# Kernel optimization log

Hardware: AMD Instinct MI355X
Metric: run time of the kernel (lower is better)

## Reference

```python
import jax, jax.numpy as jnp
import numpy as np

N, E, R = 50000, 320000, 3
IN, HID, OUT = 768, 256, 64
NEG_SLOPE = 0.2


def _rgat_conv(x, src, dst, edge_type, W, q, k, bias):
    # x: [N, HID]; W: [R, HID, HID]; q,k: [HID, 1]; bias: [HID]
    n = x.shape[0]
    xw = jnp.einsum('nc,rco->rno', x, W)          # [R, N, HID] per-relation transform
    out_i = xw[edge_type, dst]                      # [E, HID] transformed target feats
    out_j = xw[edge_type, src]                      # [E, HID] transformed source feats
    alpha = jax.nn.leaky_relu(out_i @ q + out_j @ k, NEG_SLOPE)  # [E, 1]
    # across-relation segment softmax over destination nodes (PyG softmax semantics)
    m = jax.ops.segment_max(alpha, dst, num_segments=n)          # [N, 1]
    ea = jnp.exp(alpha - m[dst])
    denom = jax.ops.segment_sum(ea, dst, num_segments=n)         # [N, 1]
    a = ea / (denom[dst] + 1e-16)                                # [E, 1]
    out = jax.ops.segment_sum(a * out_j, dst, num_segments=n)    # [N, HID]
    return out + bias


def setup_inputs() -> dict:
    key = jax.random.key(0)
    ks = jax.random.split(key, 16)
    g = lambda k, shape, fan: (jax.random.normal(k, shape, jnp.float32) / np.float32(np.sqrt(fan)))
    return {
        'x': jax.random.normal(ks[0], (N, IN), jnp.float32),
        'edge_index': jax.random.randint(ks[1], (2, E), 0, N),
        'edge_type': jax.random.randint(ks[2], (E,), 0, R),
        'w_in': g(ks[3], (IN, HID), IN), 'b_in': jnp.zeros((HID,), jnp.float32),
        'conv1_w': g(ks[4], (R, HID, HID), HID),
        'conv1_q': g(ks[5], (HID, 1), HID),
        'conv1_k': g(ks[6], (HID, 1), HID),
        'conv1_b': jnp.zeros((HID,), jnp.float32),
        'conv2_w': g(ks[7], (R, HID, HID), HID),
        'conv2_q': g(ks[8], (HID, 1), HID),
        'conv2_k': g(ks[9], (HID, 1), HID),
        'conv2_b': jnp.zeros((HID,), jnp.float32),
        'w_out': g(ks[10], (HID, OUT), HID), 'b_out': jnp.zeros((OUT,), jnp.float32),
        'w_cls': g(ks[11], (OUT, 2), OUT), 'b_cls': jnp.zeros((2,), jnp.float32),
    }


def reference(x, edge_index, edge_type, w_in, b_in,
              conv1_w, conv1_q, conv1_k, conv1_b,
              conv2_w, conv2_q, conv2_k, conv2_b,
              w_out, b_out, w_cls, b_cls):
    src, dst = edge_index[0], edge_index[1]
    h = jax.nn.relu(x @ w_in + b_in)                                  # [N, HID]
    h = _rgat_conv(h, src, dst, edge_type, conv1_w, conv1_q, conv1_k, conv1_b)
    h = _rgat_conv(h, src, dst, edge_type, conv2_w, conv2_q, conv2_k, conv2_b)
    h = jax.nn.relu(h @ w_out + b_out)                                # [N, OUT]
    return h @ w_cls + b_cls                                          # [N, 2]
```

## Files before the change

kernel.cpp:

```cpp
#include <hip/hip_runtime.h>
#include <hip/hip_bf16.h>

#define RG86_NN 50000
#define RG86_NE 320000
#define RG86_NR 3
#define RG86_DIN 768
#define RG86_HID 256
#define RG86_OUT 64

typedef __bf16 rg_bv8 __attribute__((ext_vector_type(8)));
typedef short rg_sv8 __attribute__((ext_vector_type(8)));
typedef float rg_fv4 __attribute__((ext_vector_type(4)));
typedef unsigned int rg_u32;

static __device__ float rg_b2f(unsigned short u) {
  return __uint_as_float(((unsigned int)u) << 16);
}
static __device__ unsigned short rg_f2b(float f) {
  unsigned int u = __float_as_uint(f);
  u += 0x7FFFu + ((u >> 16) & 1u);
  return (unsigned short)(u >> 16);
}

static __device__ __forceinline__ void rg_gl16(const void* g, void* lds_wave_base) {
  __builtin_amdgcn_global_load_lds(
      (const __attribute__((address_space(1))) rg_u32*)(unsigned long long)(uintptr_t)g,
      (__attribute__((address_space(3))) rg_u32*)(unsigned int)(uintptr_t)lds_wave_base,
      16, 0, 0);
}

__global__ void RGATModel_86371792322702_kernel() {}

__global__ void rg_cast(const float* in, unsigned short* out, int n) {
  int i = (blockIdx.x * 256 + threadIdx.x) * 4;
  if (i < n) {
    float4 v = *(const float4*)(in + i);
    ushort4 o = make_ushort4(rg_f2b(v.x), rg_f2b(v.y), rg_f2b(v.z), rg_f2b(v.w));
    *(ushort4*)(out + i) = o;
  }
}

__global__ void rg_castT(const float* in, unsigned short* out, int rows, int cols) {
  int i = blockIdx.x * 256 + threadIdx.x;
  if (i < rows * cols) {
    int r = i / cols, c = i % cols;
    out[(size_t)c * rows + r] = rg_f2b(in[i]);
  }
}

__global__ void rg_castT3(const float* in, unsigned short* out) {
  int i = blockIdx.x * 256 + threadIdx.x;
  if (i < RG86_NR * RG86_HID * RG86_HID) {
    int r = i >> 16, j = i & 65535;
    int row = j >> 8, col = j & 255;
    out[(r << 16) + (col << 8) + row] = rg_f2b(in[i]);
  }
}

__global__ __launch_bounds__(256) void rg_gemm2(
    const unsigned short* A, const unsigned short* Bt, const float* bias,
    unsigned short* C, int M, int N, int K, int relu, int split) {
  __shared__ unsigned short sA[128 * 64];
  __shared__ unsigned short sB[64 * 64];
  int tid = threadIdx.x;
  int wv = tid >> 6, lane = tid & 63;
  int nwg = gridDim.x;
  int q = nwg >> 3, rres = nwg & 7;
  int xcd = blockIdx.x & 7, jj = blockIdx.x >> 3;
  int wg = (xcd < rres ? xcd * (q + 1) : rres * (q + 1) + (xcd - rres) * q) + jj;
  int ntiles = N >> 6;
  int mt = wg / ntiles, nt = wg - mt * ntiles;
  int m0 = mt * 128, n0 = nt * 64;
  int frow = lane & 15, fhi = lane >> 4;
  rg_fv4 acc[2][4] = {};
  for (int k0 = 0; k0 < K; k0 += 64) {
#pragma unroll
    for (int i = 0; i < 4; i++) {
      int idx = i * 256 + tid;
      int r = idx >> 3, s = idx & 7;
      int gr = m0 + r;
      if (gr >= M) gr = M - 1;
      const unsigned short* gp = A + (size_t)gr * K + k0 + ((s ^ (r & 7)) << 3);
      rg_gl16(gp, (char*)sA + (size_t)(i * 256 + wv * 64) * 16);
    }
#pragma unroll
    for (int i = 0; i < 2; i++) {
      int idx = i * 256 + tid;
      int r = idx >> 3, s = idx & 7;
      const unsigned short* gp = Bt + (size_t)(n0 + r) * K + k0 + ((s ^ (r & 7)) << 3);
      rg_gl16(gp, (char*)sB + (size_t)(i * 256 + wv * 64) * 16);
    }
    __syncthreads();
#pragma unroll
    for (int ks = 0; ks < 2; ks++) {
      rg_bv8 af[2], bf[4];
#pragma unroll
      for (int mf = 0; mf < 2; mf++) {
        int r = wv * 32 + mf * 16 + frow;
        int slot = (ks * 4 + fhi) ^ (r & 7);
        af[mf] = *(const rg_bv8*)((const char*)sA + r * 128 + slot * 16);
      }
#pragma unroll
      for (int nf = 0; nf < 4; nf++) {
        int r = nf * 16 + frow;
        int slot = (ks * 4 + fhi) ^ (r & 7);
        bf[nf] = *(const rg_bv8*)((const char*)sB + r * 128 + slot * 16);
      }
#pragma unroll
      for (int mf = 0; mf < 2; mf++)
#pragma unroll
        for (int nf = 0; nf < 4; nf++)
          acc[mf][nf] = __builtin_amdgcn_mfma_f32_16x16x32_bf16(af[mf], bf[nf],
                                                                acc[mf][nf], 0, 0, 0);
    }
    __syncthreads();
  }
#pragma unroll
  for (int mf = 0; mf < 2; mf++) {
#pragma unroll
    for (int nf = 0; nf < 4; nf++) {
      int col = n0 + nf * 16 + frow;
      float bv = bias ? bias[col] : 0.f;
#pragma unroll
      for (int r = 0; r < 4; r++) {
        int row = m0 + wv * 32 + mf * 16 + fhi * 4 + r;
        if (row < M) {
          float v = acc[mf][nf][r] + bv;
          if (relu && v < 0.f) v = 0.f;
          if (split)
            C[((size_t)(col >> 8) * RG86_NN + row) * 256 + (col & 255)] = rg_f2b(v);
          else
            C[(size_t)row * N + col] = rg_f2b(v);
        }
      }
    }
  }
}

__global__ void rg_hist(const int* d, int* counts) {
  int e = blockIdx.x * 256 + threadIdx.x;
  if (e < RG86_NE) atomicAdd(&counts[d[e]], 1);
}

__global__ void rg_scan1(const int* counts, int* tmp, int* bsum, int n) {
  int b = blockIdx.x, t = threadIdx.x;
  int base = b * 1024 + t * 4;
  int v0 = 0, v1 = 0, v2 = 0, v3 = 0;
  if (base + 3 < n) {
    int4 v = *(const int4*)(counts + base);
    v0 = v.x; v1 = v.y; v2 = v.z; v3 = v.w;
  } else {
    if (base + 0 < n) v0 = counts[base + 0];
    if (base + 1 < n) v1 = counts[base + 1];
    if (base + 2 < n) v2 = counts[base + 2];
    if (base + 3 < n) v3 = counts[base + 3];
  }
  int tsum = v0 + v1 + v2 + v3;
  int lane = t & 63, wave = t >> 6;
  int s = tsum;
  for (int off = 1; off < 64; off <<= 1) {
    int u = __shfl_up(s, off);
    if (lane >= off) s += u;
  }
  __shared__ int wsum[4];
  if (lane == 63) wsum[wave] = s;
  __syncthreads();
  int woff = 0;
  for (int w = 0; w < wave; w++) woff += wsum[w];
  int excl = woff + s - tsum;
  int e0 = excl, e1 = e0 + v0, e2 = e1 + v1, e3 = e2 + v2;
  if (base + 3 < n) {
    *(int4*)(tmp + base) = make_int4(e0, e1, e2, e3);
  } else {
    if (base + 0 < n) tmp[base + 0] = e0;
    if (base + 1 < n) tmp[base + 1] = e1;
    if (base + 2 < n) tmp[base + 2] = e2;
    if (base + 3 < n) tmp[base + 3] = e3;
  }
  if (t == 255) bsum[b] = woff + s;
}

__global__ void rg_scan2(int* bsum, int* rowptr, int nb, int n) {
  int lane = threadIdx.x;
  int v = (lane < nb) ? bsum[lane] : 0;
  int s = v;
  for (int off = 1; off < 64; off <<= 1) {
    int u = __shfl_up(s, off);
    if (lane >= off) s += u;
  }
  if (lane < nb) bsum[lane] = s - v;
  if (lane == 63) rowptr[n] = s;
}

__global__ void rg_scan3(const int* bsum, int* rowptr, int* cursor, int n) {
  int b = blockIdx.x, t = threadIdx.x;
  int base = b * 1024 + t * 4;
  int off = bsum[b];
  if (base + 3 < n) {
    int4 v = *(const int4*)(cursor + base);
    int4 o = make_int4(v.x + off, v.y + off, v.z + off, v.w + off);
    *(int4*)(rowptr + base) = o;
    *(int4*)(cursor + base) = o;
  } else {
    for (int j = 0; j < 4; j++)
      if (base + j < n) {
        int o = cursor[base + j] + off;
        rowptr[base + j] = o;
        cursor[base + j] = o;
      }
  }
}

__global__ void rg_scatter(const int* d, int* cursor, int* perm) {
  int e = blockIdx.x * 256 + threadIdx.x;
  if (e < RG86_NE) perm[atomicAdd(&cursor[d[e]], 1)] = e;
}

__global__ void rg_qk(const unsigned short* xw, const float* q, const float* k,
                      float* qd, float* kd) {
  int lane = threadIdx.x & 63;
  int p = blockIdx.x * 4 + (threadIdx.x >> 6);
  if (p >= RG86_NR * RG86_NN) return;
  const unsigned short* xr = xw + (size_t)p * RG86_HID + lane * 4;
  float qv = 0.f, kv = 0.f;
  for (int j = 0; j < 4; j++) {
    float xv = rg_b2f(xr[j]);
    qv += xv * q[lane * 4 + j];
    kv += xv * k[lane * 4 + j];
  }
  for (int o = 32; o >= 1; o >>= 1) { qv += __shfl_xor(qv, o); kv += __shfl_xor(kv, o); }
  if (lane == 0) { qd[p] = qv; kd[p] = kv; }
}

__global__ void rg_edge(const int* perm, const int* src, const int* dst,
                        const int* et, const float* qd, const float* kd,
                        float* alphap, int* srcrel) {
  int i = blockIdx.x * 256 + threadIdx.x;
  if (i >= RG86_NE) return;
  int e = perm[i];
  int t = et[e], sv = src[e], dv = dst[e];
  float al = qd[t * RG86_NN + dv] + kd[t * RG86_NN + sv];
  al = al > 0.f ? al : 0.2f * al;
  alphap[i] = al;
  srcrel[i] = t * RG86_NN + sv;
}

__global__ void rg_agg(const int* rowptr, const float* alphap, const int* srcrel,
                       const unsigned short* xw, const float* bias,
                       unsigned short* out) {
  __shared__ float sw[4][64];
  __shared__ int ssrc[4][64];
  int lane = threadIdx.x & 63;
  int wv = threadIdx.x >> 6;
  int node = blockIdx.x * 4 + wv;
  if (node >= RG86_NN) return;
  int s0 = rowptr[node], s1 = rowptr[node + 1];
  int c0 = lane * 4;
  float a0 = 0.f, a1 = 0.f, a2 = 0.f, a3 = 0.f;
  if (s1 > s0) {
    float m = -1e30f;
    for (int bs = s0; bs < s1; bs += 64) {
      int i = bs + lane;
      float al = (i < s1) ? alphap[i] : -1e30f;
      m = fmaxf(m, al);
    }
    for (int o = 32; o >= 1; o >>= 1) m = fmaxf(m, __shfl_xor(m, o));
    float den = 0.f;
    for (int bs = s0; bs < s1; bs += 64) {
      int i = bs + lane;
      if (i < s1) den += __expf(alphap[i] - m);
    }
    for (int o = 32; o >= 1; o >>= 1) den += __shfl_xor(den, o);
    float inv = 1.f / (den + 1e-16f);
    for (int bs = s0; bs < s1; bs += 64) {
      int i = bs + lane;
      int nch = s1 - bs; if (nch > 64) nch = 64;
      float w = 0.f; int sr = 0;
      if (i < s1) { w = __expf(alphap[i] - m) * inv; sr = srcrel[i]; }
      sw[wv][lane] = w;
      ssrc[wv][lane] = sr;
#pragma unroll 4
      for (int j = 0; j < nch; j++) {
        float wj = sw[wv][j];
        ushort4 v = *(const ushort4*)(xw + (size_t)ssrc[wv][j] * RG86_HID + c0);
        a0 += wj * rg_b2f(v.x);
        a1 += wj * rg_b2f(v.y);
        a2 += wj * rg_b2f(v.z);
        a3 += wj * rg_b2f(v.w);
      }
    }
  }
  unsigned short* op = out + (size_t)node * RG86_HID + c0;
  op[0] = rg_f2b(a0 + bias[c0 + 0]);
  op[1] = rg_f2b(a1 + bias[c0 + 1]);
  op[2] = rg_f2b(a2 + bias[c0 + 2]);
  op[3] = rg_f2b(a3 + bias[c0 + 3]);
}

__global__ void rg_cls(const unsigned short* h4, const float* wc, const float* bc,
                       float* out) {
  int n = blockIdx.x * 256 + threadIdx.x;
  if (n >= RG86_NN) return;
  float a0 = bc[0], a1 = bc[1];
  const unsigned short* hr = h4 + (size_t)n * RG86_OUT;
  for (int j = 0; j < RG86_OUT; j++) {
    float h = rg_b2f(hr[j]);
    a0 += h * wc[j * 2 + 0];
    a1 += h * wc[j * 2 + 1];
  }
  out[n * 2 + 0] = a0;
  out[n * 2 + 1] = a1;
}

extern "C" void kernel_launch(void* const* d_in, const int* in_sizes, int n_in,
                              void* d_out, int out_size, void* d_ws, size_t ws_size,
                              hipStream_t stream) {
  (void)in_sizes; (void)n_in; (void)out_size;
  const float* x = (const float*)d_in[0];
  const int* ei = (const int*)d_in[1];
  const int* etp = (const int*)d_in[2];
  const float* w_in = (const float*)d_in[3];
  const float* b_in = (const float*)d_in[4];
  const float* c1w = (const float*)d_in[5];
  const float* c1q = (const float*)d_in[6];
  const float* c1k = (const float*)d_in[7];
  const float* c1b = (const float*)d_in[8];
  const float* c2w = (const float*)d_in[9];
  const float* c2q = (const float*)d_in[10];
  const float* c2k = (const float*)d_in[11];
  const float* c2b = (const float*)d_in[12];
  const float* w_out = (const float*)d_in[13];
  const float* b_out = (const float*)d_in[14];
  const float* w_cls = (const float*)d_in[15];
  const float* b_cls = (const float*)d_in[16];
  const int* esrc = ei;
  const int* edst = ei + RG86_NE;

  char* base = (char*)d_ws;
  size_t off = 0;
  unsigned short* xb = (unsigned short*)(base + off);
  unsigned short* xw = xb;
  off += (size_t)RG86_NN * RG86_DIN * 2;
  unsigned short* h1b = (unsigned short*)(base + off); off += (size_t)RG86_NN * RG86_HID * 2;
  unsigned short* h2b = (unsigned short*)(base + off); off += (size_t)RG86_NN * RG86_HID * 2;
  unsigned short* h4b = (unsigned short*)(base + off); off += (size_t)RG86_NN * RG86_OUT * 2;
  unsigned short* w_inT = (unsigned short*)(base + off); off += (size_t)RG86_DIN * RG86_HID * 2;
  unsigned short* c1wT = (unsigned short*)(base + off); off += (size_t)RG86_NR * RG86_HID * RG86_HID * 2;
  unsigned short* c2wT = (unsigned short*)(base + off); off += (size_t)RG86_NR * RG86_HID * RG86_HID * 2;
  unsigned short* w_outT = (unsigned short*)(base + off); off += (size_t)RG86_HID * RG86_OUT * 2;
  float* qd = (float*)(base + off); off += (size_t)RG86_NR * RG86_NN * 4;
  float* kd = (float*)(base + off); off += (size_t)RG86_NR * RG86_NN * 4;
  int* counts = (int*)(base + off); off += (size_t)RG86_NN * 4;
  int* rowptr = (int*)(base + off); off += (size_t)(RG86_NN + 4) * 4;
  int* cursor = (int*)(base + off); off += (size_t)RG86_NN * 4;
  int* perm = (int*)(base + off); off += (size_t)RG86_NE * 4;
  int* bsum = (int*)(base + off); off += (size_t)64 * 4;
  float* alphap = (float*)(base + off); off += (size_t)RG86_NE * 4;
  int* srcrel = (int*)(base + off); off += (size_t)RG86_NE * 4;
  if (off > ws_size) return;

  int mt128 = (RG86_NN + 127) / 128;
  int nsb = (RG86_NN + 1023) / 1024;

  rg_cast<<<(RG86_NN * RG86_DIN / 4 + 255) / 256, 256, 0, stream>>>(
      x, xb, RG86_NN * RG86_DIN);
  rg_castT<<<(RG86_DIN * RG86_HID + 255) / 256, 256, 0, stream>>>(
      w_in, w_inT, RG86_DIN, RG86_HID);
  rg_castT3<<<(RG86_NR * RG86_HID * RG86_HID + 255) / 256, 256, 0, stream>>>(c1w, c1wT);
  rg_castT3<<<(RG86_NR * RG86_HID * RG86_HID + 255) / 256, 256, 0, stream>>>(c2w, c2wT);
  rg_castT<<<(RG86_HID * RG86_OUT + 255) / 256, 256, 0, stream>>>(
      w_out, w_outT, RG86_HID, RG86_OUT);

  rg_gemm2<<<mt128 * 4, 256, 0, stream>>>(xb, w_inT, b_in, h1b,
                                          RG86_NN, RG86_HID, RG86_DIN, 1, 0);

  hipMemsetAsync(counts, 0, (size_t)RG86_NN * 4, stream);
  rg_hist<<<(RG86_NE + 255) / 256, 256, 0, stream>>>(edst, counts);
  rg_scan1<<<nsb, 256, 0, stream>>>(counts, cursor, bsum, RG86_NN);
  rg_scan2<<<1, 64, 0, stream>>>(bsum, rowptr, nsb, RG86_NN);
  rg_scan3<<<nsb, 256, 0, stream>>>(bsum, rowptr, cursor, RG86_NN);
  rg_scatter<<<(RG86_NE + 255) / 256, 256, 0, stream>>>(edst, cursor, perm);

  rg_gemm2<<<mt128 * 12, 256, 0, stream>>>(h1b, c1wT, (const float*)0, xw,
                                           RG86_NN, RG86_NR * RG86_HID, RG86_HID, 0, 1);
  rg_qk<<<(RG86_NR * RG86_NN + 3) / 4, 256, 0, stream>>>(xw, c1q, c1k, qd, kd);
  rg_edge<<<(RG86_NE + 255) / 256, 256, 0, stream>>>(perm, esrc, edst, etp, qd, kd,
                                                     alphap, srcrel);
  rg_agg<<<(RG86_NN + 3) / 4, 256, 0, stream>>>(rowptr, alphap, srcrel,
                                                xw, c1b, h2b);

  rg_gemm2<<<mt128 * 12, 256, 0, stream>>>(h2b, c2wT, (const float*)0, xw,
                                           RG86_NN, RG86_NR * RG86_HID, RG86_HID, 0, 1);
  rg_qk<<<(RG86_NR * RG86_NN + 3) / 4, 256, 0, stream>>>(xw, c2q, c2k, qd, kd);
  rg_edge<<<(RG86_NE + 255) / 256, 256, 0, stream>>>(perm, esrc, edst, etp, qd, kd,
                                                     alphap, srcrel);
  rg_agg<<<(RG86_NN + 3) / 4, 256, 0, stream>>>(rowptr, alphap, srcrel,
                                                xw, c2b, h1b);

  rg_gemm2<<<mt128, 256, 0, stream>>>(h1b, w_outT, b_out, h4b,
                                      RG86_NN, RG86_OUT, RG86_HID, 1, 0);

  rg_cls<<<(RG86_NN + 255) / 256, 256, 0, stream>>>(h4b, w_cls, b_cls, (float*)d_out);
}
```

Baseline: 586.1 us.

## Fuse input cast into first GEMM and precompute W·q, W·k projections

Removes the separate fp32-to-bf16 cast pass over x by having a new GEMM variant load fp32 A tiles, convert them in registers and store them to LDS. It also folds the attention vectors into the relation weights (W·q, W·k), so the per-node attention scores come from a 256-wide read of h rather than a read of the three-relation transformed tensor. This cuts one full read/write of the 50000x768 input and shrinks the qk pass by about 3x. In exchange, the A load is now a synchronous register path instead of an async LDS load, and the scores are computed from bf16 h with fp32 weights, which slightly changes rounding.

```diff
diff --git a/kernel.cpp b/kernel.cpp
--- a/kernel.cpp
+++ b/kernel.cpp
@@ -31,15 +31,6 @@
 
 __global__ void RGATModel_86371792322702_kernel() {}
 
-__global__ void rg_cast(const float* in, unsigned short* out, int n) {
-  int i = (blockIdx.x * 256 + threadIdx.x) * 4;
-  if (i < n) {
-    float4 v = *(const float4*)(in + i);
-    ushort4 o = make_ushort4(rg_f2b(v.x), rg_f2b(v.y), rg_f2b(v.z), rg_f2b(v.w));
-    *(ushort4*)(out + i) = o;
-  }
-}
-
 __global__ void rg_castT(const float* in, unsigned short* out, int rows, int cols) {
   int i = blockIdx.x * 256 + threadIdx.x;
   if (i < rows * cols) {
@@ -54,6 +45,49 @@
     int r = i >> 16, j = i & 65535;
     int row = j >> 8, col = j & 255;
     out[(r << 16) + (col << 8) + row] = rg_f2b(in[i]);
+  }
+}
+
+__global__ void rg_wqk(const float* W, const float* q, const float* k,
+                       float* wq, float* wk) {
+  int lane = threadIdx.x & 63;
+  int p = blockIdx.x * 4 + (threadIdx.x >> 6);
+  if (p >= RG86_NR * RG86_HID) return;
+  const float* wr = W + (size_t)p * RG86_HID;
+  float qv = 0.f, kv = 0.f;
+  for (int j = lane; j < RG86_HID; j += 64) {
+    float w = wr[j];
+    qv += w * q[j];
+    kv += w * k[j];
+  }
+  for (int o = 32; o >= 1; o >>= 1) { qv += __shfl_xor(qv, o); kv += __shfl_xor(kv, o); }
+  if (lane == 0) { wq[p] = qv; wk[p] = kv; }
+}
+
+__global__ void rg_qk2(const unsigned short* h, const float* wq, const float* wk,
+                       float* qd, float* kd) {
+  int lane = threadIdx.x & 63;
+  int n = blockIdx.x * 4 + (threadIdx.x >> 6);
+  if (n >= RG86_NN) return;
+  ushort4 hv = *(const ushort4*)(h + (size_t)n * RG86_HID + lane * 4);
+  float h0 = rg_b2f(hv.x), h1 = rg_b2f(hv.y), h2 = rg_b2f(hv.z), h3 = rg_b2f(hv.w);
+  float acc[6];
+#pragma unroll
+  for (int r = 0; r < RG86_NR; r++) {
+    const float* wqr = wq + r * RG86_HID + lane * 4;
+    const float* wkr = wk + r * RG86_HID + lane * 4;
+    acc[r] = h0 * wqr[0] + h1 * wqr[1] + h2 * wqr[2] + h3 * wqr[3];
+    acc[3 + r] = h0 * wkr[0] + h1 * wkr[1] + h2 * wkr[2] + h3 * wkr[3];
+  }
+#pragma unroll
+  for (int j = 0; j < 6; j++)
+    for (int o = 32; o >= 1; o >>= 1) acc[j] += __shfl_xor(acc[j], o);
+  if (lane == 0) {
+#pragma unroll
+    for (int r = 0; r < RG86_NR; r++) {
+      qd[r * RG86_NN + n] = acc[r];
+      kd[r * RG86_NN + n] = acc[3 + r];
+    }
   }
 }
 
@@ -137,6 +171,99 @@
   }
 }
 
+__global__ __launch_bounds__(256) void rg_gemm2f(
+    const float* A, const unsigned short* Bt, const float* bias,
+    unsigned short* C, int M, int N, int K, int relu) {
+  __shared__ unsigned short sA[128 * 64];
+  __shared__ unsigned short sB[64 * 64];
+  int tid = threadIdx.x;
+  int wv = tid >> 6, lane = tid & 63;
+  int nwg = gridDim.x;
+  int q = nwg >> 3, rres = nwg & 7;
+  int xcd = blockIdx.x & 7, jj = blockIdx.x >> 3;
+  int wg = (xcd < rres ? xcd * (q + 1) : rres * (q + 1) + (xcd - rres) * q) + jj;
+  int ntiles = N >> 6;
+  int mt = wg / ntiles, nt = wg - mt * ntiles;
+  int m0 = mt * 128, n0 = nt * 64;
+  int frow = lane & 15, fhi = lane >> 4;
+  rg_fv4 acc[2][4] = {};
+  for (int k0 = 0; k0 < K; k0 += 64) {
+#pragma unroll
+    for (int i = 0; i < 2; i++) {
+      int idx = i * 256 + tid;
+      int r = idx >> 3, s = idx & 7;
+      const unsigned short* gp = Bt + (size_t)(n0 + r) * K + k0 + ((s ^ (r & 7)) << 3);
+      rg_gl16(gp, (char*)sB + (size_t)(i * 256 + wv * 64) * 16);
+    }
+    float4 fa[4][2];
+#pragma unroll
+    for (int i = 0; i < 4; i++) {
+      int idx = i * 256 + tid;
+      int r = idx >> 3, s = idx & 7;
+      int gr = m0 + r;
+      if (gr >= M) gr = M - 1;
+      const float* gp = A + (size_t)gr * K + k0 + ((s ^ (r & 7)) << 3);
+      fa[i][0] = *(const float4*)gp;
+      fa[i][1] = *(const float4*)(gp + 4);
+    }
+#pragma unroll
+    for (int i = 0; i < 4; i++) {
+      int idx = i * 256 + tid;
+      rg_sv8 bvv;
+      bvv[0] = (short)rg_f2b(fa[i][0].x);
+      bvv[1] = (short)rg_f2b(fa[i][0].y);
+      bvv[2] = (short)rg_f2b(fa[i][0].z);
+      bvv[3] = (short)rg_f2b(fa[i][0].w);
+      bvv[4] = (short)rg_f2b(fa[i][1].x);
+      bvv[5] = (short)rg_f2b(fa[i][1].y);
+      bvv[6] = (short)rg_f2b(fa[i][1].z);
+      bvv[7] = (short)rg_f2b(fa[i][1].w);
+      *(rg_sv8*)((char*)sA + (size_t)idx * 16) = bvv;
+    }
+    __syncthreads();
+#pragma unroll
+    for (int ks = 0; ks < 2; ks++) {
+      rg_bv8 af[2], bf[4];
+#pragma unroll
+      for (int mf = 0; mf < 2; mf++) {
+        int r = wv * 32 + mf * 16 + frow;
+        int slot = (ks * 4 + fhi) ^ (r & 7);
+        af[mf] = *(const rg_bv8*)((const char*)sA + r * 128 + slot * 16);
+      }
+#pragma unroll
+      for (int nf = 0; nf < 4; nf++) {
+        int r = nf * 16 + frow;
+        int slot = (ks * 4 + fhi) ^ (r & 7);
+        bf[nf] = *(const rg_bv8*)((const char*)sB + r * 128 + slot * 16);
+      }
+#pragma unroll
+      for (int mf = 0; mf < 2; mf++)
+#pragma unroll
+        for (int nf = 0; nf < 4; nf++)
+          acc[mf][nf] = __builtin_amdgcn_mfma_f32_16x16x32_bf16(af[mf], bf[nf],
+                                                                acc[mf][nf], 0, 0, 0);
+    }
+    __syncthreads();
+  }
+#pragma unroll
+  for (int mf = 0; mf < 2; mf++) {
+#pragma unroll
+    for (int nf = 0; nf < 4; nf++) {
+      int col = n0 + nf * 16 + frow;
+      float bv = bias ? bias[col] : 0.f;
+#pragma unroll
+      for (int r = 0; r < 4; r++) {
+        int row = m0 + wv * 32 + mf * 16 + fhi * 4 + r;
+        if (row < M) {
+          float v = acc[mf][nf][r] + bv;
+          if (relu && v < 0.f) v = 0.f;
+          C[(size_t)row * N + col] = rg_f2b(v);
+        }
+      }
+    }
+  }
+}
+
 __global__ void rg_hist(const int* d, int* counts) {
   int e = blockIdx.x * 256 + threadIdx.x;
   if (e < RG86_NE) atomicAdd(&counts[d[e]], 1);
@@ -214,22 +341,6 @@
 __global__ void rg_scatter(const int* d, int* cursor, int* perm) {
   int e = blockIdx.x * 256 + threadIdx.x;
   if (e < RG86_NE) perm[atomicAdd(&cursor[d[e]], 1)] = e;
-}
-
-__global__ void rg_qk(const unsigned short* xw, const float* q, const float* k,
-                      float* qd, float* kd) {
-  int lane = threadIdx.x & 63;
-  int p = blockIdx.x * 4 + (threadIdx.x >> 6);
-  if (p >= RG86_NR * RG86_NN) return;
-  const unsigned short* xr = xw + (size_t)p * RG86_HID + lane * 4;
-  float qv = 0.f, kv = 0.f;
-  for (int j = 0; j < 4; j++) {
-    float xv = rg_b2f(xr[j]);
-    qv += xv * q[lane * 4 + j];
-    kv += xv * k[lane * 4 + j];
-  }
-  for (int o = 32; o >= 1; o >>= 1) { qv += __shfl_xor(qv, o); kv += __shfl_xor(kv, o); }
-  if (lane == 0) { qd[p] = qv; kd[p] = kv; }
 }
 
 __global__ void rg_edge(const int* perm, const int* src, const int* dst,
@@ -338,9 +449,8 @@
 
   char* base = (char*)d_ws;
   size_t off = 0;
-  unsigned short* xb = (unsigned short*)(base + off);
-  unsigned short* xw = xb;
-  off += (size_t)RG86_NN * RG86_DIN * 2;
+  unsigned short* xw = (unsigned short*)(base + off);
+  off += (size_t)RG86_NR * RG86_NN * RG86_HID * 2;
   unsigned short* h1b = (unsigned short*)(base + off); off += (size_t)RG86_NN * RG86_HID * 2;
   unsigned short* h2b = (unsigned short*)(base + off); off += (size_t)RG86_NN * RG86_HID * 2;
   unsigned short* h4b = (unsigned short*)(base + off); off += (size_t)RG86_NN * RG86_OUT * 2;
@@ -350,6 +460,10 @@
   unsigned short* w_outT = (unsigned short*)(base + off); off += (size_t)RG86_HID * RG86_OUT * 2;
   float* qd = (float*)(base + off); off += (size_t)RG86_NR * RG86_NN * 4;
   float* kd = (float*)(base + off); off += (size_t)RG86_NR * RG86_NN * 4;
+  float* wq1 = (float*)(base + off); off += (size_t)RG86_NR * RG86_HID * 4;
+  float* wk1 = (float*)(base + off); off += (size_t)RG86_NR * RG86_HID * 4;
+  float* wq2 = (float*)(base + off); off += (size_t)RG86_NR * RG86_HID * 4;
+  float* wk2 = (float*)(base + off); off += (size_t)RG86_NR * RG86_HID * 4;
   int* counts = (int*)(base + off); off += (size_t)RG86_NN * 4;
   int* rowptr = (int*)(base + off); off += (size_t)(RG86_NN + 4) * 4;
   int* cursor = (int*)(base + off); off += (size_t)RG86_NN * 4;
@@ -362,17 +476,17 @@
   int mt128 = (RG86_NN + 127) / 128;
   int nsb = (RG86_NN + 1023) / 1024;
 
-  rg_cast<<<(RG86_NN * RG86_DIN / 4 + 255) / 256, 256, 0, stream>>>(
-      x, xb, RG86_NN * RG86_DIN);
   rg_castT<<<(RG86_DIN * RG86_HID + 255) / 256, 256, 0, stream>>>(
       w_in, w_inT, RG86_DIN, RG86_HID);
   rg_castT3<<<(RG86_NR * RG86_HID * RG86_HID + 255) / 256, 256, 0, stream>>>(c1w, c1wT);
   rg_castT3<<<(RG86_NR * RG86_HID * RG86_HID + 255) / 256, 256, 0, stream>>>(c2w, c2wT);
   rg_castT<<<(RG86_HID * RG86_OUT + 255) / 256, 256, 0, stream>>>(
       w_out, w_outT, RG86_HID, RG86_OUT);
-
-  rg_gemm2<<<mt128 * 4, 256, 0, stream>>>(xb, w_inT, b_in, h1b,
-                                          RG86_NN, RG86_HID, RG86_DIN, 1, 0);
+  rg_wqk<<<(RG86_NR * RG86_HID + 3) / 4, 256, 0, stream>>>(c1w, c1q, c1k, wq1, wk1);
+  rg_wqk<<<(RG86_NR * RG86_HID + 3) / 4, 256, 0, stream>>>(c2w, c2q, c2k, wq2, wk2);
+
+  rg_gemm2f<<<mt128 * 4, 256, 0, stream>>>(x, w_inT, b_in, h1b,
+                                           RG86_NN, RG86_HID, RG86_DIN, 1);
 
   hipMemsetAsync(counts, 0, (size_t)RG86_NN * 4, stream);
   rg_hist<<<(RG86_NE + 255) / 256, 256, 0, stream>>>(edst, counts);
@@ -383,7 +497,7 @@
 
   rg_gemm2<<<mt128 * 12, 256, 0, stream>>>(h1b, c1wT, (const float*)0, xw,
                                            RG86_NN, RG86_NR * RG86_HID, RG86_HID, 0, 1);
-  rg_qk<<<(RG86_NR * RG86_NN + 3) / 4, 256, 0, stream>>>(xw, c1q, c1k, qd, kd);
+  rg_qk2<<<(RG86_NN + 3) / 4, 256, 0, stream>>>(h1b, wq1, wk1, qd, kd);
   rg_edge<<<(RG86_NE + 255) / 256, 256, 0, stream>>>(perm, esrc, edst, etp, qd, kd,
                                                      alphap, srcrel);
   rg_agg<<<(RG86_NN + 3) / 4, 256, 0, stream>>>(rowptr, alphap, srcrel,
@@ -391,7 +505,7 @@
 
   rg_gemm2<<<mt128 * 12, 256, 0, stream>>>(h2b, c2wT, (const float*)0, xw,
                                            RG86_NN, RG86_NR * RG86_HID, RG86_HID, 0, 1);
-  rg_qk<<<(RG86_NR * RG86_NN + 3) / 4, 256, 0, stream>>>(xw, c2q, c2k, qd, kd);
+  rg_qk2<<<(RG86_NN + 3) / 4, 256, 0, stream>>>(h2b, wq2, wk2, qd, kd);
   rg_edge<<<(RG86_NE + 255) / 256, 256, 0, stream>>>(perm, esrc, edst, etp, qd, kd,
                                                      alphap, srcrel);
   rg_agg<<<(RG86_NN + 3) / 4, 256, 0, stream>>>(rowptr, alphap, srcrel,
```

Result: slower. 622.7 us (+6.2%).
